# Kernel optimization log

Measured on AMD Instinct MI355X. Metric: run time of the kernel, lower is better.

Reference implementation:

```python
import jax, jax.numpy as jnp
import numpy as np

B, D, H, S = 32, 512, 256, 131072
CAP_LIMIT, MIN_NOV, STORE_TH, ACT_TH = 0.85, 0.4, 0.35, 0.5
STAB_TARGET = 0.1

def _lin(x, w, b):
    return x @ w.T + b

def _ln(x, g, b):
    m = x.mean(-1, keepdims=True)
    v = ((x - m) ** 2).mean(-1, keepdims=True)
    return (x - m) / jnp.sqrt(v + 1e-5) * g + b

def _l2n(x):
    return x / jnp.clip(jnp.linalg.norm(x, axis=-1, keepdims=True), 1e-12)

def _forward(new_content, query, memory_bank, access_times,
             rel_w1, rel_b1, rel_g, rel_bb, rel_w2, rel_b2,
             nov_w, nov_b, gate_w, gate_b,
             lru_w, lru_b, conf_w, conf_b, eg_w, eg_b,
             dd_w1, dd_b1, dd_w2, dd_b2,
             ds_w1, ds_b1, ds_w2, ds_b2,
             decay_rate, memory_change_ema, current_step):
    step = jnp.float32(current_step)
    mem0 = memory_bank
    capacity = jnp.float32((jnp.linalg.norm(mem0, axis=-1) > ACT_TH).sum()) / S
    # ---- store gating ----
    combined = jnp.concatenate([new_content, query], axis=-1)                 # [B, 2D]
    rel = jax.nn.relu(_lin(jax.nn.relu(_ln(_lin(combined, rel_w1, rel_b1), rel_g, rel_bb)), rel_w2, rel_b2))
    sims = _l2n(new_content) @ _l2n(mem0).T                                   # [B, S]
    max_sim = sims.max(axis=-1, keepdims=True)
    novelty = (1.0 - max_sim) / 2.0
    nov_feat = jax.nn.sigmoid(_lin(new_content, nov_w, nov_b))
    store_score = jax.nn.sigmoid(_lin(rel + nov_feat, gate_w, gate_b))        # [B,1]
    base_store = store_score.mean() > STORE_TH
    novelty_ok = novelty.mean() > MIN_NOV
    should_store = jnp.logical_and(base_store, novelty_ok)
    over_cap = capacity > CAP_LIMIT
    # ---- emergency erase (applied only when over capacity) ----
    age = jnp.maximum(step - access_times, 0.0)
    erase_sc0 = age / (age.max() + 1e-6) + (1.0 - jax.nn.sigmoid(jnp.linalg.norm(mem0, axis=-1)))
    victim = jnp.argmax(erase_sc0)
    mem = mem0.at[victim].set(jnp.where(over_cap, 0.0, mem0[victim]))
    at = access_times.at[victim].set(jnp.where(over_cap, -99999.0, access_times[victim]))
    # ---- learned erase scores ----
    lru = jax.nn.relu(_lin(((step - at) / 1000.0)[:, None], lru_w, lru_b))    # [S, 32]
    conf = jax.nn.sigmoid(_lin(mem, conf_w, conf_b))                          # [S, 32]
    erase_scores = jax.nn.sigmoid(_lin(jnp.concatenate([lru, conf], -1), eg_w, eg_b))[:, 0]
    # ---- conflict detection + drift (sequential masked scatter, faithful order) ----
    sims2 = _l2n(new_content) @ _l2n(mem).T                                   # [B, S]
    topv, topi = jax.lax.top_k(sims2, 3)                                      # [B, 3]
    conflict_mask = jnp.logical_and(topv > 0.7, topv < 0.99)
    old = mem[topi]                                                           # [B, 3, D]
    newb = jnp.broadcast_to(new_content[:, None, :], (B, 3, D))
    pair = jnp.concatenate([newb, old], axis=-1)                              # [B, 3, 2D]
    prob = jax.nn.sigmoid(_lin(jax.nn.relu(_lin(pair, dd_w1, dd_b1)), dd_w2, dd_b2))[..., 0]
    strength = jax.nn.sigmoid(_lin(jax.nn.relu(_lin(pair, ds_w1, ds_b1)), ds_w2, ds_b2))
    avg = (newb + old) / 2.0
    cand_new = (1.0 - strength) * newb + strength * avg
    cand_old = (1.0 - strength) * old + strength * avg
    active = jnp.logical_and(conflict_mask, prob > 0.5).reshape(-1)           # [B*3]
    fi = topi.reshape(-1)
    fn = cand_new.reshape(B * 3, D)
    fo = cand_old.reshape(B * 3, D)
    def body(i, carry):
        dn, do = carry
        b = i // 3
        s = fi[i]
        dn = dn.at[b].set(jnp.where(active[i], fn[i], dn[b]))
        do = do.at[s].set(jnp.where(active[i], fo[i], do[s]))
        return dn, do
    drifted_new, mem = jax.lax.fori_loop(0, B * 3, body, (new_content, mem))
    # ---- conditional store (no-grad write in original) ----
    write_idx = jnp.where(over_cap, victim, jnp.argmax(erase_scores))
    mem = mem.at[write_idx].set(jnp.where(should_store, jax.lax.stop_gradient(drifted_new[0]), mem[write_idx]))
    at = at.at[write_idx].set(jnp.where(should_store, step, at[write_idx]))
    # ---- stability / plasticity decay update ----
    change = jnp.abs(mem - mem0).mean()
    ema_new = 0.9 * memory_change_ema + 0.1 * change
    adjustment = jnp.where(ema_new.sum() > STAB_TARGET, -0.005, 0.005)
    decay_new = jnp.clip(decay_rate + adjustment, 0.01, 0.2)
    relevance = jax.nn.sigmoid(max_sim).mean()
    return (mem, at, erase_scores, store_score.mean(), novelty.mean(), relevance,
            capacity, conflict_mask.sum().astype(jnp.float32), decay_new, ema_new)

def setup_inputs() -> dict:
    key = jax.random.key(0)
    ks = iter(jax.random.split(key, 40))
    def rn(*shape):
        return jax.random.normal(next(ks), shape, dtype=jnp.float32) * 0.02
    return dict(
        new_content=jax.random.normal(next(ks), (B, D), dtype=jnp.float32),
        query=jax.random.normal(next(ks), (B, D), dtype=jnp.float32),
        memory_bank=jax.random.normal(next(ks), (S, D), dtype=jnp.float32),
        access_times=jax.random.uniform(next(ks), (S,), dtype=jnp.float32) * 1000.0,
        rel_w1=rn(H, 2 * D), rel_b1=jnp.zeros((H,)), rel_g=jnp.ones((H,)), rel_bb=jnp.zeros((H,)),
        rel_w2=rn(H // 2, H), rel_b2=jnp.zeros((H // 2,)),
        nov_w=rn(H // 2, D), nov_b=jnp.zeros((H // 2,)),
        gate_w=rn(1, H // 2), gate_b=jnp.zeros((1,)),
        lru_w=rn(32, 1), lru_b=jnp.zeros((32,)),
        conf_w=rn(32, D), conf_b=jnp.zeros((32,)),
        eg_w=rn(1, 64), eg_b=jnp.zeros((1,)),
        dd_w1=rn(H, 2 * D), dd_b1=jnp.zeros((H,)), dd_w2=rn(1, H), dd_b2=jnp.zeros((1,)),
        ds_w1=rn(H, 2 * D), ds_b1=jnp.zeros((H,)), ds_w2=rn(1, H), ds_b2=jnp.zeros((1,)),
        decay_rate=jnp.float32(0.04),
        memory_change_ema=jnp.zeros((1,), dtype=jnp.float32),
        current_step=5000,
    )

def reference(new_content, query, memory_bank, access_times,
              rel_w1, rel_b1, rel_g, rel_bb, rel_w2, rel_b2,
              nov_w, nov_b, gate_w, gate_b,
              lru_w, lru_b, conf_w, conf_b, eg_w, eg_b,
              dd_w1, dd_b1, dd_w2, dd_b2,
              ds_w1, ds_b1, ds_w2, ds_b2,
              decay_rate, memory_change_ema, current_step):
    return _forward(new_content, query, memory_bank, access_times,
                    rel_w1, rel_b1, rel_g, rel_bb, rel_w2, rel_b2,
                    nov_w, nov_b, gate_w, gate_b,
                    lru_w, lru_b, conf_w, conf_b, eg_w, eg_b,
                    dd_w1, dd_b1, dd_w2, dd_b2,
                    ds_w1, ds_b1, ds_w2, ds_b2,
                    decay_rate, memory_change_ema, current_step)
```

## Files before the change

### kernel.cpp

```cpp
#include <hip/hip_runtime.h>
#include <math.h>

typedef unsigned int u32;
typedef unsigned long long u64;

#define S_N 131072
#define OUT_AT   67108864L
#define OUT_ES   67239936L
#define OUT_SC   67371008L

#define W_WCT   0L
#define W_NORM2 32768L
#define W_CER   163840L
#define W_T4V   294912L
#define W_T4I   557056L
#define W_ATOM  819200L
#define W_FLAG  819208L
#define W_T3V   819216L
#define W_T3I   819312L
#define W_MAXS  819408L
#define W_ACT   819440L
#define W_CN    819536L
#define W_CO    868688L

__device__ __forceinline__ float sigm(float x){ return 1.0f/(1.0f + expf(-x)); }

__global__ __launch_bounds__(256) void k0(
    const float* __restrict__ nc, const float* __restrict__ query,
    const float* __restrict__ at_in,
    const float* __restrict__ rel_w1, const float* __restrict__ rel_b1,
    const float* __restrict__ rel_g, const float* __restrict__ rel_bb,
    const float* __restrict__ rel_w2, const float* __restrict__ rel_b2,
    const float* __restrict__ nov_w, const float* __restrict__ nov_b,
    const float* __restrict__ gate_w, const float* __restrict__ gate_b,
    const float* __restrict__ conf_w,
    const int* __restrict__ stepp,
    float* __restrict__ ws)
{
  const int bid = blockIdx.x, t = threadIdx.x;
  if (bid < 32) {
    __shared__ __align__(16) float scomb[1024];
    __shared__ __align__(16) float shr[256];
    __shared__ float red[256];
    const float* ncb = nc + bid*512;
    const float* qb  = query + bid*512;
    for (int i=t;i<1024;i+=256) scomb[i] = (i<512)? ncb[i] : qb[i-512];
    __syncthreads();
    float p = scomb[t]*scomb[t] + scomb[t+256]*scomb[t+256];
    red[t]=p; __syncthreads();
    for (int o=128;o>0;o>>=1){ if(t<o) red[t]+=red[t+o]; __syncthreads(); }
    const float denom = fmaxf(sqrtf(red[0]), 1e-12f);
    __syncthreads();
    float* wct = ws + W_WCT;
    wct[(long)t*64 + bid]       = scomb[t]/denom;
    wct[(long)(t+256)*64 + bid] = scomb[t+256]/denom;
    const float4* w1r = (const float4*)(rel_w1 + (long)t*1024);
    const float4* sc4 = (const float4*)scomb;
    float a1 = rel_b1[t];
    #pragma unroll 4
    for (int k=0;k<256;k++){ float4 w=w1r[k], s=sc4[k]; a1 += w.x*s.x+w.y*s.y+w.z*s.z+w.w*s.w; }
    red[t]=a1; __syncthreads();
    for (int o=128;o>0;o>>=1){ if(t<o) red[t]+=red[t+o]; __syncthreads(); }
    const float mean = red[0]/256.0f;
    __syncthreads();
    const float dd = a1-mean;
    red[t]=dd*dd; __syncthreads();
    for (int o=128;o>0;o>>=1){ if(t<o) red[t]+=red[t+o]; __syncthreads(); }
    const float var = red[0]/256.0f;
    __syncthreads();
    const float xh = (a1-mean)/sqrtf(var+1e-5f);
    shr[t] = fmaxf(xh*rel_g[t]+rel_bb[t], 0.0f);
    __syncthreads();
    float gp = 0.0f;
    if (t<128){
      const float4* w2r = (const float4*)(rel_w2 + (long)t*256);
      const float4* sh4 = (const float4*)shr;
      float a2 = rel_b2[t];
      #pragma unroll 4
      for (int k=0;k<64;k++){ float4 w=w2r[k], s=sh4[k]; a2 += w.x*s.x+w.y*s.y+w.z*s.z+w.w*s.w; }
      const float relv = fmaxf(a2,0.0f);
      const float4* nwr = (const float4*)(nov_w + (long)t*512);
      float a3 = nov_b[t];
      #pragma unroll 4
      for (int k=0;k<128;k++){ float4 w=nwr[k], s=sc4[k]; a3 += w.x*s.x+w.y*s.y+w.z*s.z+w.w*s.w; }
      gp = (relv + sigm(a3))*gate_w[t];
    }
    red[t]=gp; __syncthreads();
    for (int o=128;o>0;o>>=1){ if(t<o) red[t]+=red[t+o]; __syncthreads(); }
    if (t==0) atomicAdd((float*)(ws+W_ATOM+6), sigm(red[0]+gate_b[0]));
  } else if (bid < 64) {
    const int j = bid-32;
    float* wct = ws + W_WCT;
    for (int k=t;k<512;k+=256) wct[(long)k*64 + 32 + j] = conf_w[j*512+k];
  } else {
    __shared__ float red[256];
    const float step = (float)(*stepp);
    const int per = (S_N + 191)/192;
    const int base = (bid-64)*per;
    const int end = min(base+per, S_N);
    float m = 0.0f;
    for (int s=base+t; s<end; s+=256) m = fmaxf(m, fmaxf(step - at_in[s], 0.0f));
    red[t]=m; __syncthreads();
    for (int o=128;o>0;o>>=1){ if(t<o) red[t]=fmaxf(red[t],red[t+o]); __syncthreads(); }
    if (t==0) atomicMax((u32*)(ws+W_ATOM+0), __float_as_uint(red[0]));
  }
}

__global__ __launch_bounds__(256,3) void k1(
    const float* __restrict__ mem,
    const float* __restrict__ conf_b, const float* __restrict__ eg_w,
    float* __restrict__ out, float* __restrict__ ws)
{
  __shared__ __align__(16) float lx[64*68];
  __shared__ __align__(16) float lw[16*276];
  __shared__ float ssim[64][33];
  __shared__ float snorm[64];
  const int t = threadIdx.x, bid = blockIdx.x;
  const long rowbase = (long)bid*64;
  const int lane = t & 63;
  const int hr = t >> 4;
  const int cj = t & 15;
  const int c4 = cj*4;
  const int q = t & 3, c16 = (t>>2)&3, r4 = t>>4;
  const int swz = r4 & 3;
  const float* wct = ws + W_WCT;
  float acc[4][16];
  #pragma unroll
  for (int i=0;i<4;i++){
    #pragma unroll
    for (int m=0;m<16;m++) acc[i][m]=0.0f;
  }
  float normp[4] = {0.0f,0.0f,0.0f,0.0f};
  #pragma unroll 1
  for (int ch=0; ch<8; ++ch) {
    #pragma unroll
    for (int it=0; it<4; ++it) {
      const int r = 16*it + hr;
      const long g = (rowbase + r)*512 + ch*64 + c4;
      float4 v = *(const float4*)(mem + g);
      *(float4*)(out + g) = v;
      const int cjs = cj ^ ((r>>2)&3);
      *(float4*)&lx[r*68 + cjs*4] = v;
      normp[it] += v.x*v.x + v.y*v.y + v.z*v.z + v.w*v.w;
    }
    #pragma unroll
    for (int it=0; it<4; ++it) {
      float4 v = *(const float4*)(wct + (long)(ch*64 + 16*it + hr)*64 + c4);
      *(float4*)&lw[hr*276 + it*68 + c4] = v;
    }
    __syncthreads();
    #pragma unroll
    for (int kk4=0; kk4<4; ++kk4) {
      float xa[4][4];
      #pragma unroll
      for (int i=0;i<4;i++){
        float4 v = *(const float4*)&lx[(r4*4+i)*68 + (((q*4+kk4)^swz)*4)];
        xa[i][0]=v.x; xa[i][1]=v.y; xa[i][2]=v.z; xa[i][3]=v.w;
      }
      #pragma unroll
      for (int e=0;e<4;e++){
        const float* wp = &lw[(kk4*4+e)*276 + q*68 + c16*16];
        float4 w0 = *(const float4*)(wp);
        float4 w1 = *(const float4*)(wp+4);
        float4 w2 = *(const float4*)(wp+8);
        float4 w3 = *(const float4*)(wp+12);
        #pragma unroll
        for (int i=0;i<4;i++){
          const float xs = xa[i][e];
          acc[i][0]+=xs*w0.x; acc[i][1]+=xs*w0.y; acc[i][2]+=xs*w0.z; acc[i][3]+=xs*w0.w;
          acc[i][4]+=xs*w1.x; acc[i][5]+=xs*w1.y; acc[i][6]+=xs*w1.z; acc[i][7]+=xs*w1.w;
          acc[i][8]+=xs*w2.x; acc[i][9]+=xs*w2.y; acc[i][10]+=xs*w2.z; acc[i][11]+=xs*w2.w;
          acc[i][12]+=xs*w3.x; acc[i][13]+=xs*w3.y; acc[i][14]+=xs*w3.z; acc[i][15]+=xs*w3.w;
        }
      }
    }
    __syncthreads();
  }
  #pragma unroll
  for (int it=0; it<4; ++it) {
    float v = normp[it];
    v += __shfl_xor(v,8); v += __shfl_xor(v,4); v += __shfl_xor(v,2); v += __shfl_xor(v,1);
    if ((lane & 15)==0) snorm[16*it + hr] = v;
  }
  __syncthreads();
  #pragma unroll
  for (int i=0;i<4;i++){
    #pragma unroll
    for (int m=0;m<16;m++){
      float v = acc[i][m];
      v += __shfl_xor(v,1);
      v += __shfl_xor(v,2);
      acc[i][m]=v;
    }
  }
  if (q==0){
    if (c16<2){
      #pragma unroll
      for (int i=0;i<4;i++){
        const int R = r4*4+i;
        const float inv = 1.0f/fmaxf(sqrtf(snorm[R]),1e-12f);
        #pragma unroll
        for (int m=0;m<16;m++) ssim[R][c16*16+m] = acc[i][m]*inv;
      }
    } else {
      #pragma unroll
      for (int i=0;i<4;i++){
        float part=0.0f;
        #pragma unroll
        for (int m=0;m<16;m++){
          const int j=(c16-2)*16+m;
          part += eg_w[32+j]*sigm(acc[i][m]+conf_b[j]);
        }
        part += __shfl_xor(part,4);
        if (c16==2) (ws+W_CER)[rowbase + r4*4+i]=part;
      }
    }
  }
  if (t<64) (ws+W_NORM2)[rowbase + t] = snorm[t];
  __syncthreads();
  if (t==0) {
    u32 c=0;
    for (int r=0;r<64;r++) c += (sqrtf(snorm[r]) > 0.5f)?1u:0u;
    atomicAdd((u32*)(ws+W_ATOM+1), c);
  }
  if (t<32) {
    float v0=-2,v1=-2,v2=-2,v3=-2; int i0=0,i1=0,i2=0,i3=0;
    for (int r=0;r<64;r++){
      const float v = ssim[r][t]; const int gi = (int)rowbase + r;
      if (v > v2) {
        if (v > v0)      { v3=v2;i3=i2; v2=v1;i2=i1; v1=v0;i1=i0; v0=v;i0=gi; }
        else if (v > v1) { v3=v2;i3=i2; v2=v1;i2=i1; v1=v;i1=gi; }
        else             { v3=v2;i3=i2; v2=v;i2=gi; }
      } else if (v > v3) { v3=v;i3=gi; }
    }
    float* t4v = ws + W_T4V + (long)t*8192 + bid*4;
    int*   t4i = (int*)(ws + W_T4I) + (long)t*8192 + bid*4;
    t4v[0]=v0; t4v[1]=v1; t4v[2]=v2; t4v[3]=v3;
    t4i[0]=i0; t4i[1]=i1; t4i[2]=i2; t4i[3]=i3;
  }
}

__global__ __launch_bounds__(256) void kv2(
    const float* __restrict__ at_in, const int* __restrict__ stepp,
    float* __restrict__ ws, float* __restrict__ out)
{
  __shared__ u64 red[256];
  const int t = threadIdx.x, bid = blockIdx.x;
  if (bid==0 && t==0) {
    const u32 cnt = *(u32*)(ws+W_ATOM+1);
    const float cap = (float)cnt / (float)S_N;
    out[OUT_SC+3] = cap;
    ((int*)(ws+W_FLAG))[0] = (cap > 0.85f) ? 1 : 0;
  }
  const float step = (float)(*stepp);
  const float agemax = __uint_as_float(*(u32*)(ws+W_ATOM+0));
  const float dnm = agemax + 1e-6f;
  const float* n2 = ws+W_NORM2;
  const int base = bid*512;
  u64 best = 0;
  #pragma unroll
  for (int i=0;i<2;i++) {
    const int s = base + t + i*256;
    const float age = fmaxf(step - at_in[s], 0.0f);
    const float q = age/dnm;
    const float nr = sqrtf(n2[s]);
    const float sc = q + (1.0f - sigm(nr));
    const u64 key = ((u64)__float_as_uint(sc)<<32) | (u64)(0xFFFFFFFFu - (u32)s);
    best = (key>best)?key:best;
  }
  red[t]=best; __syncthreads();
  for (int o=128;o>0;o>>=1){ if(t<o){ u64 a=red[t],b2=red[t+o]; red[t]=(a>b2)?a:b2; } __syncthreads(); }
  if (t==0) atomicMax((u64*)(ws+W_ATOM+2), red[0]);
}

__device__ __forceinline__ void ins3(float v, int idx, float* V, int* I){
  if ( (v>V[0]) || (v==V[0] && idx<I[0]) ) { V[2]=V[1];I[2]=I[1]; V[1]=V[0];I[1]=I[0]; V[0]=v;I[0]=idx; }
  else if ( (v>V[1]) || (v==V[1] && idx<I[1]) ) { V[2]=V[1];I[2]=I[1]; V[1]=v;I[1]=idx; }
  else if ( (v>V[2]) || (v==V[2] && idx<I[2]) ) { V[2]=v;I[2]=idx; }
}

__global__ __launch_bounds__(256) void k3m(
    const float* __restrict__ at_in, const int* __restrict__ stepp,
    const float* __restrict__ lru_w, const float* __restrict__ lru_b,
    const float* __restrict__ eg_w, const float* __restrict__ eg_b,
    const float* __restrict__ conf_b,
    float* __restrict__ ws, float* __restrict__ out)
{
  __shared__ u64 red[256];
  __shared__ float lv[768];
  __shared__ int   li[768];
  __shared__ float lm[256];
  const int t=threadIdx.x, bid=blockIdx.x;
  const u64 vk = *(u64*)(ws+W_ATOM+2);
  const int victim = (int)(0xFFFFFFFFu - (u32)(vk & 0xFFFFFFFFull));
  const int oc = ((int*)(ws+W_FLAG))[0];
  if (bid < 256) {
    if (bid==0 && t==0) ((int*)(ws+W_FLAG))[1] = victim;
    const float step = (float)(*stepp);
    float* at_out = out + OUT_AT;
    float* es_out = out + OUT_ES;
    const float* cer = ws+W_CER;
    u64 best=0;
    const int base=bid*512;
    for (int i=0;i<2;i++){
      const int s = base + t + i*256;
      const float a = at_in[s];
      const bool isv = oc && (s==victim);
      const float av = isv ? -99999.0f : a;
      at_out[s] = av;
      const float x = (step - av)/1000.0f;
      float lsum = 0.0f;
      #pragma unroll
      for (int j=0;j<32;j++) lsum += eg_w[j]*fmaxf(lru_w[j]*x + lru_b[j], 0.0f);
      float ce;
      if (isv) { ce=0.0f; for (int j=0;j<32;j++) ce += eg_w[32+j]*sigm(conf_b[j]); }
      else ce = cer[s];
      const float es = sigm(lsum + ce + eg_b[0]);
      es_out[s] = es;
      const u64 key = ((u64)__float_as_uint(es)<<32) | (u64)(0xFFFFFFFFu - (u32)s);
      best = (key>best)?key:best;
    }
    red[t]=best; __syncthreads();
    for (int o=128;o>0;o>>=1){ if(t<o){ u64 a=red[t],b2=red[t+o]; red[t]=(a>b2)?a:b2; } __syncthreads(); }
    if (t==0) atomicMax((u64*)(ws+W_ATOM+4), red[0]);
  } else {
    const int b = bid - 256;
    const float* t4v = ws + W_T4V + (long)b*8192;
    const int*   t4i = (const int*)(ws + W_T4I) + (long)b*8192;
    float V[3] = {-2,-2,-2}; int I[3] = {0,0,0};
    float mx = -2.0f;
    for (int c=t; c<8192; c+=256) {
      const float v = t4v[c];
      const int idx = t4i[c];
      if ((c&3)==0) mx = fmaxf(mx, v);
      if (oc && idx==victim) continue;
      ins3(v, idx, V, I);
    }
    lv[t*3]=V[0]; lv[t*3+1]=V[1]; lv[t*3+2]=V[2];
    li[t*3]=I[0]; li[t*3+1]=I[1]; li[t*3+2]=I[2];
    lm[t]=mx;
    __syncthreads();
    for (int off=128; off>=1; off>>=1){
      if (t<off){
        float A0=lv[t*3],A1=lv[t*3+1],A2=lv[t*3+2];
        int   B0=li[t*3],B1=li[t*3+1],B2=li[t*3+2];
        float AV[3]={A0,A1,A2}; int AI[3]={B0,B1,B2};
        ins3(lv[(t+off)*3+0], li[(t+off)*3+0], AV, AI);
        ins3(lv[(t+off)*3+1], li[(t+off)*3+1], AV, AI);
        ins3(lv[(t+off)*3+2], li[(t+off)*3+2], AV, AI);
        lv[t*3]=AV[0]; lv[t*3+1]=AV[1]; lv[t*3+2]=AV[2];
        li[t*3]=AI[0]; li[t*3+1]=AI[1]; li[t*3+2]=AI[2];
        lm[t]=fmaxf(lm[t], lm[t+off]);
      }
      __syncthreads();
    }
    if (t==0) {
      float FV[3]={lv[0],lv[1],lv[2]}; int FI[3]={li[0],li[1],li[2]};
      if (oc) ins3(0.0f, victim, FV, FI);
      for (int p=0;p<3;p++){ (ws+W_T3V)[b*3+p]=FV[p]; ((int*)(ws+W_T3I))[b*3+p]=FI[p]; }
      (ws+W_MAXS)[b]=lm[0];
    }
  }
}

__global__ __launch_bounds__(256) void k4(
    const float* __restrict__ mem, const float* __restrict__ nc,
    const float* __restrict__ dd_w1, const float* __restrict__ dd_b1,
    const float* __restrict__ dd_w2, const float* __restrict__ dd_b2,
    const float* __restrict__ ds_w1, const float* __restrict__ ds_b1,
    const float* __restrict__ ds_w2, const float* __restrict__ ds_b2,
    float* __restrict__ ws, float* __restrict__ out)
{
  const int bid = blockIdx.x, t = threadIdx.x;
  const int oc = ((int*)(ws+W_FLAG))[0];
  const int victim = ((int*)(ws+W_FLAG))[1];
  if (bid == 96) {
    if (t==0) {
      const float sm = (ws+W_ATOM)[6] / 32.0f;
      float nsum=0.0f, rsum=0.0f, csum=0.0f;
      for (int b2=0;b2<32;b2++){
        const float ms = (ws+W_MAXS)[b2];
        nsum += (1.0f-ms)/2.0f;
        rsum += sigm(ms);
      }
      for (int c=0;c<96;c++){
        const float v=(ws+W_T3V)[c];
        if (v>0.7f && v<0.99f) csum += 1.0f;
      }
      const float novm = nsum/32.0f;
      out[OUT_SC+0]=sm;
      out[OUT_SC+1]=novm;
      out[OUT_SC+2]=rsum/32.0f;
      out[OUT_SC+4]=csum;
      ((int*)(ws+W_FLAG))[2] = (sm>0.35f && novm>0.4f) ? 1 : 0;
      const u64 ek = *(u64*)(ws+W_ATOM+4);
      const int esidx = (int)(0xFFFFFFFFu - (u32)(ek & 0xFFFFFFFFull));
      ((int*)(ws+W_FLAG))[3] = oc ? victim : esidx;
    }
    return;
  }
  __shared__ __align__(16) float sp[1024];
  __shared__ __align__(16) float sh[256];
  __shared__ float red[256];
  const int b = bid/3;
  const int oi = ((int*)(ws+W_T3I))[bid];
  const float tv = (ws+W_T3V)[bid];
  const bool zold = oc && (oi==victim);
  for (int i=t;i<1024;i+=256)
    sp[i] = (i<512) ? nc[b*512+i] : (zold ? 0.0f : mem[(long)oi*512 + (i-512)]);
  __syncthreads();
  const float4* sp4 = (const float4*)sp;
  {
    const float4* wr = (const float4*)(dd_w1 + (long)t*1024);
    float a = dd_b1[t];
    #pragma unroll 4
    for (int k=0;k<256;k++){ float4 w=wr[k], s=sp4[k]; a += w.x*s.x+w.y*s.y+w.z*s.z+w.w*s.w; }
    sh[t]=fmaxf(a,0.0f);
  }
  __syncthreads();
  red[t]=sh[t]*dd_w2[t]; __syncthreads();
  for (int o=128;o>0;o>>=1){ if(t<o) red[t]+=red[t+o]; __syncthreads(); }
  const float prob = sigm(red[0]+dd_b2[0]);
  __syncthreads();
  {
    const float4* wr = (const float4*)(ds_w1 + (long)t*1024);
    float a = ds_b1[t];
    #pragma unroll 4
    for (int k=0;k<256;k++){ float4 w=wr[k], s=sp4[k]; a += w.x*s.x+w.y*s.y+w.z*s.z+w.w*s.w; }
    sh[t]=fmaxf(a,0.0f);
  }
  __syncthreads();
  red[t]=sh[t]*ds_w2[t]; __syncthreads();
  for (int o=128;o>0;o>>=1){ if(t<o) red[t]+=red[t+o]; __syncthreads(); }
  const float sstr = sigm(red[0]+ds_b2[0]);
  if (t==0) ((int*)(ws+W_ACT))[bid] = ((tv>0.7f) && (tv<0.99f) && (prob>0.5f)) ? 1 : 0;
  for (int k=t;k<512;k+=256){
    const float nw=sp[k], od=sp[512+k];
    const float avg=(nw+od)/2.0f;
    (ws+W_CN)[(long)bid*512+k] = (1.0f-sstr)*nw + sstr*avg;
    (ws+W_CO)[(long)bid*512+k] = (1.0f-sstr)*od + sstr*avg;
  }
}

__global__ __launch_bounds__(256) void k5(
    const float* __restrict__ mem, const float* __restrict__ nc,
    const float* __restrict__ decay_in, const float* __restrict__ ema_in,
    const int* __restrict__ stepp,
    float* __restrict__ ws, float* __restrict__ out)
{
  __shared__ int rows[256];
  __shared__ int nrows_s;
  __shared__ float red[256];
  const int t=threadIdx.x;
  const int oc=((int*)(ws+W_FLAG))[0];
  const int victim=((int*)(ws+W_FLAG))[1];
  const int should=((int*)(ws+W_FLAG))[2];
  const int widx=((int*)(ws+W_FLAG))[3];
  const int* act=(const int*)(ws+W_ACT);
  const int* t3i=(const int*)(ws+W_T3I);
  const float step=(float)(*stepp);
  float* at_out = out+OUT_AT;
  if (oc) { for (int k=t;k<512;k+=256) out[(long)victim*512+k]=0.0f; }
  __threadfence(); __syncthreads();
  for (int i=0;i<96;i++){
    if (act[i]) {
      const long s=t3i[i];
      for (int k=t;k<512;k+=256) out[s*512+k]=(ws+W_CO)[(long)i*512+k];
    }
  }
  int dn_src=-1;
  for (int i=0;i<3;i++) if (act[i]) dn_src=i;
  __threadfence(); __syncthreads();
  if (should) {
    for (int k=t;k<512;k+=256)
      out[(long)widx*512+k] = (dn_src>=0)? (ws+W_CN)[(long)dn_src*512+k] : nc[k];
    if (t==0) at_out[widx]=step;
  }
  __threadfence(); __syncthreads();
  if (t==0){
    int n=0;
    if (oc) rows[n++]=victim;
    for (int i=0;i<96;i++) if (act[i]) {
      const int s=t3i[i]; bool dup=false;
      for (int j=0;j<n;j++) if (rows[j]==s) dup=true;
      if (!dup) rows[n++]=s;
    }
    if (should) {
      bool dup=false;
      for (int j=0;j<n;j++) if (rows[j]==widx) dup=true;
      if (!dup) rows[n++]=widx;
    }
    nrows_s=n;
  }
  __syncthreads();
  float part=0.0f;
  for (int ri=0;ri<nrows_s;ri++){
    const long base=(long)rows[ri]*512;
    for (int k=t;k<512;k+=256) part += fabsf(out[base+k]-mem[base+k]);
  }
  red[t]=part; __syncthreads();
  for (int o=128;o>0;o>>=1){ if(t<o) red[t]+=red[t+o]; __syncthreads(); }
  if (t==0){
    const float change = red[0]/67108864.0f;
    const float ema = 0.9f*ema_in[0] + 0.1f*change;
    const float adj = (ema>0.1f)? -0.005f : 0.005f;
    const float dec = fminf(fmaxf(decay_in[0]+adj,0.01f),0.2f);
    out[OUT_SC+5]=dec;
    out[OUT_SC+6]=ema;
  }
}

extern "C" void kernel_launch(void* const* d_in, const int* in_sizes, int n_in,
                              void* d_out, int out_size, void* d_ws, size_t ws_size,
                              hipStream_t stream) {
  const float* nc     = (const float*)d_in[0];
  const float* query  = (const float*)d_in[1];
  const float* mem    = (const float*)d_in[2];
  const float* at_in  = (const float*)d_in[3];
  const float* rel_w1 = (const float*)d_in[4];
  const float* rel_b1 = (const float*)d_in[5];
  const float* rel_g  = (const float*)d_in[6];
  const float* rel_bb = (const float*)d_in[7];
  const float* rel_w2 = (const float*)d_in[8];
  const float* rel_b2 = (const float*)d_in[9];
  const float* nov_w  = (const float*)d_in[10];
  const float* nov_b  = (const float*)d_in[11];
  const float* gate_w = (const float*)d_in[12];
  const float* gate_b = (const float*)d_in[13];
  const float* lru_w  = (const float*)d_in[14];
  const float* lru_b  = (const float*)d_in[15];
  const float* conf_w = (const float*)d_in[16];
  const float* conf_b = (const float*)d_in[17];
  const float* eg_w   = (const float*)d_in[18];
  const float* eg_b   = (const float*)d_in[19];
  const float* dd_w1  = (const float*)d_in[20];
  const float* dd_b1  = (const float*)d_in[21];
  const float* dd_w2  = (const float*)d_in[22];
  const float* dd_b2  = (const float*)d_in[23];
  const float* ds_w1  = (const float*)d_in[24];
  const float* ds_b1  = (const float*)d_in[25];
  const float* ds_w2  = (const float*)d_in[26];
  const float* ds_b2  = (const float*)d_in[27];
  const float* decay  = (const float*)d_in[28];
  const float* ema    = (const float*)d_in[29];
  const int*   stepp  = (const int*)d_in[30];
  float* out = (float*)d_out;
  float* ws  = (float*)d_ws;

  hipMemsetAsync((char*)d_ws + (size_t)W_ATOM*4, 0, 32, stream);

  k0 <<<dim3(256), dim3(256), 0, stream>>>(nc, query, at_in, rel_w1, rel_b1, rel_g, rel_bb,
                                           rel_w2, rel_b2, nov_w, nov_b, gate_w, gate_b,
                                           conf_w, stepp, ws);
  k1 <<<dim3(2048), dim3(256), 0, stream>>>(mem, conf_b, eg_w, out, ws);
  kv2<<<dim3(256), dim3(256), 0, stream>>>(at_in, stepp, ws, out);
  k3m<<<dim3(288), dim3(256), 0, stream>>>(at_in, stepp, lru_w, lru_b, eg_w, eg_b, conf_b, ws, out);
  k4 <<<dim3(97),  dim3(256), 0, stream>>>(mem, nc, dd_w1, dd_b1, dd_w2, dd_b2,
                                           ds_w1, ds_b1, ds_w2, ds_b2, ws, out);
  k5 <<<dim3(1),   dim3(256), 0, stream>>>(mem, nc, decay, ema, stepp, ws, out);
}
```

Before: 414.2 us.

## Double-buffer k1 LDS tiles and prefetch next chunk into registers

Restructures the k1 main loop so shared-memory tiles for the memory-bank rows and weights are double-buffered, and the next chunk's global loads go into registers before the current chunk's compute. This hides global-load latency behind the FMA work and removes one barrier per chunk. It costs more LDS and registers, so launch bounds drop from 3 to 2 blocks per CU, which lowers occupancy. The ssim/snorm buffers are aliased onto the union buffer and the barrier is moved to keep that aliasing safe.

```diff
diff --git a/kernel.cpp b/kernel.cpp
--- a/kernel.cpp
+++ b/kernel.cpp
@@ -106,15 +106,19 @@
   }
 }
 
-__global__ __launch_bounds__(256,3) void k1(
+__global__ __launch_bounds__(256,2) void k1(
     const float* __restrict__ mem,
     const float* __restrict__ conf_b, const float* __restrict__ eg_w,
     float* __restrict__ out, float* __restrict__ ws)
 {
-  __shared__ __align__(16) float lx[64*68];
-  __shared__ __align__(16) float lw[16*276];
-  __shared__ float ssim[64][33];
-  __shared__ float snorm[64];
+  __shared__ __align__(16) float SM[17536];
+  float* const lxA = SM;
+  float* const lxB = SM + 4352;
+  float* const lwA = SM + 8704;
+  float* const lwB = SM + 13120;
+  float* const ssim  = SM;
+  float* const snorm = SM + 2112;
+
   const int t = threadIdx.x, bid = blockIdx.x;
   const long rowbase = (long)bid*64;
   const int lane = t & 63;
@@ -124,6 +128,7 @@
   const int q = t & 3, c16 = (t>>2)&3, r4 = t>>4;
   const int swz = r4 & 3;
   const float* wct = ws + W_WCT;
+
   float acc[4][16];
   #pragma unroll
   for (int i=0;i<4;i++){
@@ -131,24 +136,33 @@
     for (int m=0;m<16;m++) acc[i][m]=0.0f;
   }
   float normp[4] = {0.0f,0.0f,0.0f,0.0f};
-  #pragma unroll 1
-  for (int ch=0; ch<8; ++ch) {
+  float4 xv[4], wv[4];
+
+  #pragma unroll
+  for (int it=0;it<4;++it){
+    xv[it] = *(const float4*)(mem + (rowbase + 16*it + hr)*512 + c4);
+    wv[it] = *(const float4*)(wct + (long)(16*it + hr)*64 + c4);
+  }
+
+  auto stage = [&](float* lx, float* lw, int ch){
     #pragma unroll
-    for (int it=0; it<4; ++it) {
+    for (int it=0;it<4;++it){
       const int r = 16*it + hr;
-      const long g = (rowbase + r)*512 + ch*64 + c4;
-      float4 v = *(const float4*)(mem + g);
-      *(float4*)(out + g) = v;
-      const int cjs = cj ^ ((r>>2)&3);
-      *(float4*)&lx[r*68 + cjs*4] = v;
+      float4 v = xv[it];
+      *(float4*)(out + (rowbase + r)*512 + ch*64 + c4) = v;
       normp[it] += v.x*v.x + v.y*v.y + v.z*v.z + v.w*v.w;
-    }
+      *(float4*)&lx[r*68 + (cj ^ ((r>>2)&3))*4] = v;
+      *(float4*)&lw[hr*276 + it*68 + c4] = wv[it];
+    }
+  };
+  auto prefetch = [&](int ch){
     #pragma unroll
-    for (int it=0; it<4; ++it) {
-      float4 v = *(const float4*)(wct + (long)(ch*64 + 16*it + hr)*64 + c4);
-      *(float4*)&lw[hr*276 + it*68 + c4] = v;
-    }
-    __syncthreads();
+    for (int it=0;it<4;++it){
+      xv[it] = *(const float4*)(mem + (rowbase + 16*it + hr)*512 + ch*64 + c4);
+      wv[it] = *(const float4*)(wct + (long)(ch*64 + 16*it + hr)*64 + c4);
+    }
+  };
+  auto compute = [&](const float* lx, const float* lw){
     #pragma unroll
     for (int kk4=0; kk4<4; ++kk4) {
       float xa[4][4];
@@ -174,15 +188,26 @@
         }
       }
     }
-    __syncthreads();
-  }
+  };
+
+  #pragma unroll 1
+  for (int ch=0; ch<8; ch+=2){
+    stage(lxA, lwA, ch);
+    __syncthreads();
+    prefetch(ch+1);
+    compute(lxA, lwA);
+    stage(lxB, lwB, ch+1);
+    __syncthreads();
+    if (ch+2<8) prefetch(ch+2);
+    compute(lxB, lwB);
+  }
+
   #pragma unroll
   for (int it=0; it<4; ++it) {
     float v = normp[it];
     v += __shfl_xor(v,8); v += __shfl_xor(v,4); v += __shfl_xor(v,2); v += __shfl_xor(v,1);
     if ((lane & 15)==0) snorm[16*it + hr] = v;
   }
-  __syncthreads();
   #pragma unroll
   for (int i=0;i<4;i++){
     #pragma unroll
@@ -193,6 +218,7 @@
       acc[i][m]=v;
     }
   }
+  __syncthreads();
   if (q==0){
     if (c16<2){
       #pragma unroll
@@ -200,7 +226,7 @@
         const int R = r4*4+i;
         const float inv = 1.0f/fmaxf(sqrtf(snorm[R]),1e-12f);
         #pragma unroll
-        for (int m=0;m<16;m++) ssim[R][c16*16+m] = acc[i][m]*inv;
+        for (int m=0;m<16;m++) ssim[R*33 + c16*16+m] = acc[i][m]*inv;
       }
     } else {
       #pragma unroll
@@ -226,7 +252,7 @@
   if (t<32) {
     float v0=-2,v1=-2,v2=-2,v3=-2; int i0=0,i1=0,i2=0,i3=0;
     for (int r=0;r<64;r++){
-      const float v = ssim[r][t]; const int gi = (int)rowbase + r;
+      const float v = ssim[r*33 + t]; const int gi = (int)rowbase + r;
       if (v > v2) {
         if (v > v0)      { v3=v2;i3=i2; v2=v1;i2=i1; v1=v0;i1=i0; v0=v;i0=gi; }
         else if (v > v1) { v3=v2;i3=i2; v2=v1;i2=i1; v1=v;i1=gi; }
@@ -342,9 +368,8 @@
     __syncthreads();
     for (int off=128; off>=1; off>>=1){
       if (t<off){
-        float A0=lv[t*3],A1=lv[t*3+1],A2=lv[t*3+2];
-        int   B0=li[t*3],B1=li[t*3+1],B2=li[t*3+2];
-        float AV[3]={A0,A1,A2}; int AI[3]={B0,B1,B2};
+        float AV[3]={lv[t*3],lv[t*3+1],lv[t*3+2]};
+        int   AI[3]={li[t*3],li[t*3+1],li[t*3+2]};
         ins3(lv[(t+off)*3+0], li[(t+off)*3+0], AV, AI);
         ins3(lv[(t+off)*3+1], li[(t+off)*3+1], AV, AI);
         ins3(lv[(t+off)*3+2], li[(t+off)*3+2], AV, AI);
```

After: 1.156 ms. 2.79x slower.
